# Optimization experiments

Hardware: AMD Instinct MI355X
Metric: run time of the kernel (lower is better)

## Reference

```python
import jax, jax.numpy as jnp
import numpy as np

IMSIZE = 128; R = 2; B = 2; C = 3; D = 64; Q = 128; M = 8; ITERS = 32
N = IMSIZE * IMSIZE
EPS = 1e-8


def _build_edges(S, r):
    # local (2r+1)^2 pixel neighborhood, as in build_perception(imsize, perception_size)
    ys, xs = np.meshgrid(np.arange(S), np.arange(S), indexing='ij')
    rows, cols = [], []
    for dy in range(-r, r + 1):
        for dx in range(-r, r + 1):
            ny, nx = ys + dy, xs + dx
            ok = (ny >= 0) & (ny < S) & (nx >= 0) & (nx < S)
            rows.append((ys * S + xs)[ok])
            cols.append((ny * S + nx)[ok])
    return (np.concatenate(rows).astype(np.int32), np.concatenate(cols).astype(np.int32))


def _conv(x, w, b=None):
    y = jax.lax.conv_general_dilated(x, w, (1, 1), 'SAME', dimension_numbers=('NHWC', 'HWIO', 'NHWC'))
    return y if b is None else y + b


def _bn(x, g, b):
    mu = x.mean((0, 1, 2))
    var = x.var((0, 1, 2))
    return (x - mu) * jax.lax.rsqrt(var + 1e-5) * g + b


def _resblock(f, w1, g1, t1, w2, g2, t2):
    h = jax.nn.relu(_bn(_conv(f, w1), g1, t1))
    h = _bn(_conv(h, w2), g2, t2)
    return jax.nn.relu(f + h)


def _forward(x, w_bb1, b_bb1, w_bb2, b_bb2,
             w_k1, g_k1, t_k1, w_k2, g_k2, t_k2, w_kp, b_kp,
             w_q1, g_q1, t_q1, w_q2, g_q2, t_q2, w_qp,
             h0, row, col, agent_idx):
    # conv backbone (preserves spatial resolution)
    f = jax.nn.relu(_conv(x, w_bb1, b_bb1))
    f = jax.nn.relu(_conv(f, w_bb2, b_bb2))
    # key / query heads: ResidualBlock + 1x1 conv
    ks = _conv(_resblock(f, w_k1, g_k1, t_k1, w_k2, g_k2, t_k2), w_kp, b_kp).reshape(B, N, D)
    qs = _conv(_resblock(f, w_q1, g_q1, t_q1, w_q2, g_q2, t_q2), w_qp).reshape(B, N, D)
    # edge-gather cosine similarity (torch.cosine_similarity with eps=1e-8)
    qe = qs[:, row]          # [B, E, D]
    ke = ks[:, col]          # [B, E, D]
    weights = (qe * ke).sum(-1) / (
        jnp.maximum(jnp.linalg.norm(qe, axis=-1), EPS) *
        jnp.maximum(jnp.linalg.norm(ke, axis=-1), EPS))   # [B, E]

    # 32-iteration sparse adjacency propagation: h <- normalize(A @ h)
    def step(h, _):
        msg = jnp.zeros_like(h).at[:, row, :].add(weights[:, :, None] * h[:, col, :])
        h = msg / jnp.maximum(jnp.linalg.norm(msg, axis=-1, keepdims=True), EPS)
        return h, None

    h, _ = jax.lax.scan(step, h0, None, length=ITERS)     # [B, N, Q]

    # competition routing: pixels compete for M agent slots via cosine affinity
    pix = h / jnp.maximum(jnp.linalg.norm(h, axis=-1, keepdims=True), EPS)
    ag = pix[:, agent_idx]                                # [B, M, Q]
    sim = jnp.einsum('bnq,bmq->bnm', pix, ag)
    masks = jax.nn.softmax(sim * 10.0, axis=-1)           # [B, N, M]
    return masks.reshape(B, IMSIZE, IMSIZE, M).transpose(0, 3, 1, 2)  # [B, M, W, H]


def setup_inputs() -> dict:
    key = jax.random.key(0)
    k = jax.random.split(key, 12)
    s = 0.05
    row, col = _build_edges(IMSIZE, R)
    agent_idx = np.linspace(0, N - 1, M).astype(np.int32)
    return dict(
        x=jax.random.normal(k[0], (B, IMSIZE, IMSIZE, C), jnp.float32),
        w_bb1=jax.random.normal(k[1], (3, 3, C, D), jnp.float32) * s, b_bb1=jnp.zeros((D,), jnp.float32),
        w_bb2=jax.random.normal(k[2], (3, 3, D, D), jnp.float32) * s, b_bb2=jnp.zeros((D,), jnp.float32),
        w_k1=jax.random.normal(k[3], (3, 3, D, D), jnp.float32) * s,
        g_k1=jnp.ones((D,), jnp.float32), t_k1=jnp.zeros((D,), jnp.float32),
        w_k2=jax.random.normal(k[4], (3, 3, D, D), jnp.float32) * s,
        g_k2=jnp.ones((D,), jnp.float32), t_k2=jnp.zeros((D,), jnp.float32),
        w_kp=jax.random.normal(k[5], (1, 1, D, D), jnp.float32) * s, b_kp=jnp.zeros((D,), jnp.float32),
        w_q1=jax.random.normal(k[6], (3, 3, D, D), jnp.float32) * s,
        g_q1=jnp.ones((D,), jnp.float32), t_q1=jnp.zeros((D,), jnp.float32),
        w_q2=jax.random.normal(k[7], (3, 3, D, D), jnp.float32) * s,
        g_q2=jnp.ones((D,), jnp.float32), t_q2=jnp.zeros((D,), jnp.float32),
        w_qp=jax.random.normal(k[8], (1, 1, D, D), jnp.float32) * s,
        h0=jax.random.normal(k[9], (B, N, Q), jnp.float32),
        row=jnp.asarray(row), col=jnp.asarray(col),
        agent_idx=jnp.asarray(agent_idx),
    )


def reference(x, w_bb1, b_bb1, w_bb2, b_bb2,
              w_k1, g_k1, t_k1, w_k2, g_k2, t_k2, w_kp, b_kp,
              w_q1, g_q1, t_q1, w_q2, g_q2, t_q2, w_qp,
              h0, row, col, agent_idx):
    return _forward(x, w_bb1, b_bb1, w_bb2, b_bb2,
                    w_k1, g_k1, t_k1, w_k2, g_k2, t_k2, w_kp, b_kp,
                    w_q1, g_q1, t_q1, w_q2, g_q2, t_q2, w_qp,
                    h0, row, col, agent_idx)
```

## Files before the change

### kernel.cpp

```cpp
#include <hip/hip_runtime.h>
#include <math.h>

#define NPIX 16384
#define EPSF 1e-8f

typedef float f32x4 __attribute__((ext_vector_type(4)));
typedef short s16x8 __attribute__((ext_vector_type(8)));

__device__ __forceinline__ float wred64(float s){
  s += __shfl_xor(s, 32); s += __shfl_xor(s, 16); s += __shfl_xor(s, 8);
  s += __shfl_xor(s, 4);  s += __shfl_xor(s, 2);  s += __shfl_xor(s, 1);
  return s;
}
__device__ __forceinline__ float rdlane(float v, int l){
  return __int_as_float(__builtin_amdgcn_readlane(__float_as_int(v), l));
}
__device__ __forceinline__ float dot4f(float4 a, float4 b, float acc){
  acc = fmaf(a.x,b.x,acc); acc = fmaf(a.y,b.y,acc);
  acc = fmaf(a.z,b.z,acc); acc = fmaf(a.w,b.w,acc);
  return acc;
}
__device__ __forceinline__ void bf16split(float v, unsigned short &hi, unsigned short &lo){
  unsigned u = __float_as_uint(v);
  unsigned r = u + 0x7FFFu + ((u >> 16) & 1u);
  hi = (unsigned short)(r >> 16);
  float hf = __uint_as_float(((unsigned)hi) << 16);
  float l = v - hf;
  unsigned u2 = __float_as_uint(l);
  unsigned r2 = u2 + 0x7FFFu + ((u2 >> 16) & 1u);
  lo = (unsigned short)(r2 >> 16);
}

__global__ __launch_bounds__(256) void prep_kernel(const float* __restrict__ w_bb2, const float* __restrict__ w_k1,
                            const float* __restrict__ w_k2, const float* __restrict__ w_q1,
                            const float* __restrict__ w_q2, const float* __restrict__ w_kp,
                            const float* __restrict__ w_qp, unsigned short* __restrict__ wh,
                            unsigned short* __restrict__ wl, float* __restrict__ wtp,
                            float* __restrict__ stats){
  int gid = blockIdx.x*256 + threadIdx.x;
  if (gid < 184320){
    int j = gid & 7;
    int t1 = gid >> 3;
    int lane = t1 & 63;
    int t2 = t1 >> 6;
    int kb = t2 % 18;
    int t3 = t2 / 18;
    int ct = t3 & 3;
    int c  = t3 >> 2;
    const float* src = c==0? w_bb2 : c==1? w_k1 : c==2? w_k2 : c==3? w_q1 : w_q2;
    int cout = ct*16 + (lane & 15);
    int k = kb*32 + (lane>>4)*8 + j;
    float v = src[k*64 + cout];
    unsigned short h,l; bf16split(v,h,l);
    wh[gid] = h; wl[gid] = l;
  } else if (gid < 192512){
    int t = gid - 184320; int which = t >> 12; int d = t & 4095;
    const float* src = which ? w_qp : w_kp;
    int k = d & 3, cout = (d>>2) & 63, cin4 = d >> 8;
    wtp[t] = src[(cin4*4 + k)*64 + cout];
  } else if (gid < 193024){
    stats[gid - 192512] = 0.f;
  }
}

__global__ __launch_bounds__(256) void conv1_kernel(const float* __restrict__ x, const float* __restrict__ w,
                                                    const float* __restrict__ bias, float* __restrict__ out){
  int wv = blockIdx.x*4 + (threadIdx.x >> 6);
  int c  = threadIdx.x & 63;
  int p0 = wv << 3;
  int ub = __builtin_amdgcn_readfirstlane(p0);
  int b  = ub >> 14; int i0 = ub & (NPIX-1);
  int y  = i0 >> 7, x0 = i0 & 127;
  float wv_[9][3];
  #pragma unroll
  for (int t=0;t<9;++t)
    #pragma unroll
    for (int ci=0;ci<3;++ci) wv_[t][ci] = w[(t*3+ci)*64 + c];
  float bv = bias[c];
  float acc[8];
  #pragma unroll
  for (int p=0;p<8;++p) acc[p] = bv;
  for (int ky=0; ky<3; ++ky){
    int ny = y + ky - 1;
    if ((unsigned)ny >= 128u) continue;
    const float* rowp = x + ((b<<14) + ny*128)*3;
    for (int kx=0; kx<3; ++kx){
      int t = ky*3 + kx;
      #pragma unroll
      for (int p=0;p<8;++p){
        int col = x0 + p + kx - 1;
        if ((unsigned)col < 128u){
          const float* ip = rowp + col*3;
          acc[p] = fmaf(ip[0], wv_[t][0], acc[p]);
          acc[p] = fmaf(ip[1], wv_[t][1], acc[p]);
          acc[p] = fmaf(ip[2], wv_[t][2], acc[p]);
        }
      }
    }
  }
  float* op = out + (p0 << 6) + c;
  #pragma unroll
  for (int p=0;p<8;++p) op[p*64] = fmaxf(acc[p], 0.f);
}

__global__ __launch_bounds__(512) void conv3m_kernel(const float* __restrict__ in,
    const unsigned short* __restrict__ wh, const unsigned short* __restrict__ wl,
    const float* __restrict__ bias, int relu,
    const float* __restrict__ bnst, const float* __restrict__ bng, const float* __restrict__ bnb,
    float* __restrict__ out){
  __shared__ unsigned short lhi[12672];
  __shared__ unsigned short llo[12672];
  __shared__ float lout[4352];
  __shared__ float la[64], lb[64];
  int blk = blockIdx.x;
  int xh = blk & 1, y = (blk>>1) & 127, b = blk >> 8;
  int x0 = xh << 6;
  int tid = threadIdx.x;
  if (tid < 64){
    float a = 1.f, bo = 0.f;
    if (bnst){
      float mu  = bnst[tid] * (1.f/32768.f);
      float var = bnst[64+tid] * (1.f/32768.f) - mu*mu;
      a  = bng[tid] * rsqrtf(var + 1e-5f);
      bo = bnb[tid] - mu*a;
    }
    la[tid] = a; lb[tid] = bo;
  }
  __syncthreads();
  for (int s = tid; s < 3168; s += 512){
    int pr = s >> 4, cq = s & 15;
    int ky = pr / 66, px = pr - ky*66;
    int ny = y + ky - 1, gx = x0 - 1 + px;
    float v0=0.f, v1=0.f, v2=0.f, v3=0.f;
    if ((unsigned)ny < 128u && (unsigned)gx < 128u){
      const float* ip = in + (((b<<14) + ny*128 + gx)<<6) + (cq<<2);
      float4 t = *(const float4*)ip;
      int c0 = cq<<2;
      v0 = fmaxf(fmaf(t.x, la[c0],   lb[c0]),   0.f);
      v1 = fmaxf(fmaf(t.y, la[c0+1], lb[c0+1]), 0.f);
      v2 = fmaxf(fmaf(t.z, la[c0+2], lb[c0+2]), 0.f);
      v3 = fmaxf(fmaf(t.w, la[c0+3], lb[c0+3]), 0.f);
    }
    unsigned short h0,l0,h1,l1,h2,l2,h3,l3;
    bf16split(v0,h0,l0); bf16split(v1,h1,l1); bf16split(v2,h2,l2); bf16split(v3,h3,l3);
    int slot = (cq >> 1) ^ (pr & 7);
    int byte = pr*128 + (slot<<4) + ((cq & 1) << 3);
    *(uint2*)((char*)lhi + byte) = make_uint2((unsigned)h0 | ((unsigned)h1<<16),
                                              (unsigned)h2 | ((unsigned)h3<<16));
    *(uint2*)((char*)llo + byte) = make_uint2((unsigned)l0 | ((unsigned)l1<<16),
                                              (unsigned)l2 | ((unsigned)l3<<16));
  }
  __syncthreads();
  int lane = tid & 63, wid = tid >> 6;
  int pxsub = wid & 3, ch = wid >> 2;
  int col16 = lane & 15, kgrp = lane >> 4;
  f32x4 acc0 = {0.f,0.f,0.f,0.f}, acc1 = acc0, acl0 = acc0, acl1 = acc0;
  int abase = (ch*2*18)*512 + lane*8;
  #pragma unroll
  for (int kb=0; kb<18; ++kb){
    int tap = kb >> 1;
    int ky = (tap >= 6) ? 2 : (tap >= 3 ? 1 : 0);
    int kx = tap - ky*3;
    int pr = ky*66 + pxsub*16 + col16 + kx;
    int ci0 = ((kb & 1) << 5) + (kgrp << 3);
    int byte = pr*128 + ((((ci0 >> 3) ^ (pr & 7))) << 4);
    s16x8 Bh = *(const s16x8*)((const char*)lhi + byte);
    s16x8 Bl = *(const s16x8*)((const char*)llo + byte);
    int ao = abase + kb*512;
    s16x8 Ah0 = *(const s16x8*)(wh + ao);
    s16x8 Al0 = *(const s16x8*)(wl + ao);
    s16x8 Ah1 = *(const s16x8*)(wh + ao + 9216);
    s16x8 Al1 = *(const s16x8*)(wl + ao + 9216);
    acc0 = __builtin_amdgcn_mfma_f32_16x16x32_bf16(Ah0, Bh, acc0, 0, 0, 0);
    acl0 = __builtin_amdgcn_mfma_f32_16x16x32_bf16(Ah0, Bl, acl0, 0, 0, 0);
    acc1 = __builtin_amdgcn_mfma_f32_16x16x32_bf16(Ah1, Bh, acc1, 0, 0, 0);
    acl1 = __builtin_amdgcn_mfma_f32_16x16x32_bf16(Ah1, Bl, acl1, 0, 0, 0);
    acl0 = __builtin_amdgcn_mfma_f32_16x16x32_bf16(Al0, Bh, acl0, 0, 0, 0);
    acl1 = __builtin_amdgcn_mfma_f32_16x16x32_bf16(Al1, Bh, acl1, 0, 0, 0);
  }
  acc0 = acc0 + acl0;
  acc1 = acc1 + acl1;
  int pxl = pxsub*16 + col16;
  int co0 = ch*32 + kgrp*4;
  *(f32x4*)(lout + pxl*68 + co0)      = acc0;
  *(f32x4*)(lout + pxl*68 + co0 + 16) = acc1;
  __syncthreads();
  {
    int px = tid >> 3, c8 = (tid & 7) << 3;
    const float* lp = lout + px*68 + c8;
    float r0[8];
    #pragma unroll
    for (int j=0;j<8;++j) r0[j] = lp[j];
    if (bias){
      #pragma unroll
      for (int j=0;j<8;++j) r0[j] += bias[c8+j];
    }
    if (relu){
      #pragma unroll
      for (int j=0;j<8;++j) r0[j] = fmaxf(r0[j], 0.f);
    }
    float* op = out + (((b<<14) + y*128 + x0 + px)<<6) + c8;
    #pragma unroll
    for (int j=0;j<8;++j) op[j] = r0[j];
  }
}

__global__ __launch_bounds__(256) void stats_kernel(const float* __restrict__ t, float* __restrict__ stats){
  __shared__ float s1[64], s2[64];
  int tid = threadIdx.x;
  if (tid < 64){ s1[tid] = 0.f; s2[tid] = 0.f; }
  __syncthreads();
  int gid = blockIdx.x*256 + tid;
  float sum = 0.f, ss = 0.f;
  for (int idx = gid; idx < 2097152; idx += 131072){
    float v = t[idx]; sum += v; ss += v*v;
  }
  int c = gid & 63;
  atomicAdd(&s1[c], sum);
  atomicAdd(&s2[c], ss);
  __syncthreads();
  if (tid < 64){ atomicAdd(&stats[tid], s1[tid]); atomicAdd(&stats[64+tid], s2[tid]); }
}

__global__ __launch_bounds__(256) void resfuse_kernel(float* __restrict__ t, const float* __restrict__ f,
                                                      const float* __restrict__ stats, const float* __restrict__ g,
                                                      const float* __restrict__ beta){
  int idx4 = blockIdx.x*256 + threadIdx.x;
  float4 v = ((float4*)t)[idx4];
  float4 fv = ((const float4*)f)[idx4];
  int c0 = (idx4 & 15) * 4;
  float a[4], bb[4];
  #pragma unroll
  for (int j=0;j<4;++j){
    int c = c0 + j;
    float mu  = stats[c]    * (1.f/32768.f);
    float var = stats[64+c] * (1.f/32768.f) - mu*mu;
    a[j]  = g[c] * rsqrtf(var + 1e-5f);
    bb[j] = beta[c] - mu*a[j];
  }
  v.x = fmaxf(fv.x + fmaf(v.x, a[0], bb[0]), 0.f);
  v.y = fmaxf(fv.y + fmaf(v.y, a[1], bb[1]), 0.f);
  v.z = fmaxf(fv.z + fmaf(v.z, a[2], bb[2]), 0.f);
  v.w = fmaxf(fv.w + fmaf(v.w, a[3], bb[3]), 0.f);
  ((float4*)t)[idx4] = v;
}

__global__ __launch_bounds__(256) void proj_kernel(const float* __restrict__ r, const float* __restrict__ wt1,
                                                   const float* __restrict__ bias, float* __restrict__ out,
                                                   float* __restrict__ nrm){
  int wv = blockIdx.x*4 + (threadIdx.x >> 6);
  int c  = threadIdx.x & 63;
  int p0 = wv << 3;
  int ub = __builtin_amdgcn_readfirstlane(p0);
  const float4* wq = (const float4*)wt1 + c;
  float4 w[16];
  #pragma unroll
  for (int q=0;q<16;++q) w[q] = wq[q*64];
  float bv = bias ? bias[c] : 0.f;
  #pragma unroll
  for (int p=0;p<8;++p){
    const float* ip = r + ((ub + p) << 6);
    float a0 = bv, a1 = 0.f;
    #pragma unroll
    for (int q=0;q<16;q+=2){
      float4 i0 = *(const float4*)(ip + (q<<2));
      float4 i1 = *(const float4*)(ip + ((q+1)<<2));
      a0 = dot4f(i0, w[q],   a0);
      a1 = dot4f(i1, w[q+1], a1);
    }
    float acc = a0 + a1;
    out[((p0+p)<<6) + c] = acc;
    float s = wred64(acc*acc);
    if (c == 0) nrm[p0+p] = sqrtf(s);
  }
}

#define EW_PAD 68
__global__ __launch_bounds__(256) void edge_kernel(const float* __restrict__ qs, const float* __restrict__ ks,
                                                   const float* __restrict__ nq, const float* __restrict__ nk,
                                                   float* __restrict__ W){
  __shared__ float klds[100*EW_PAD];
  __shared__ float qlds[16*EW_PAD];
  int blk = blockIdx.x;
  int b = blk >> 10; int rem = blk & 1023;
  int y = rem >> 3; int x0 = (rem & 7) << 4;
  int tid = threadIdx.x;
  for (int s = tid; s < 1600; s += 256){
    int cin4 = s & 15; int col = (s >> 4) % 20; int r = (s >> 4) / 20;
    int ry = y - 2 + r; ry = ry < 0 ? 0 : (ry > 127 ? 127 : ry);
    int cx = x0 - 2 + col; cx = cx < 0 ? 0 : (cx > 127 ? 127 : cx);
    float4 v = *(const float4*)(ks + (((b<<14) + ry*128 + cx)<<6) + cin4*4);
    *(float4*)(klds + (r*20+col)*EW_PAD + cin4*4) = v;
  }
  {
    int cin4 = tid & 15; int px = tid >> 4;
    float4 v = *(const float4*)(qs + (((b<<14) + y*128 + x0 + px)<<6) + cin4*4);
    *(float4*)(qlds + px*EW_PAD + cin4*4) = v;
  }
  __syncthreads();
  #pragma unroll
  for (int pair=0; pair<2; ++pair){
    int t2 = tid + pair*256;
    int px = t2 >> 5; int o = t2 & 31;
    if (o < 25){
      int dy = o/5 - 2, dx = o%5 - 2;
      int yy = y + dy, xx = x0 + px + dx;
      bool valid = ((unsigned)yy < 128u) && ((unsigned)xx < 128u);
      const float* kq = klds + ((dy+2)*20 + (px+dx+2))*EW_PAD;
      const float* qq = qlds + px*EW_PAD;
      float a0 = 0.f, a1 = 0.f;
      #pragma unroll
      for (int q=0; q<16; q+=2){
        a0 = dot4f(*(const float4*)(qq + q*4),     *(const float4*)(kq + q*4),     a0);
        a1 = dot4f(*(const float4*)(qq + (q+1)*4), *(const float4*)(kq + (q+1)*4), a1);
      }
      float acc = a0 + a1;
      int gp = (b<<14) + y*128 + x0 + px;
      float wv_ = 0.f;
      if (valid){
        int gj = (b<<14) + yy*128 + xx;
        float rq = 1.f / fmaxf(nq[gp], EPSF);
        float rk = 1.f / fmaxf(nk[gj], EPSF);
        wv_ = acc * rq * rk;
      }
      W[gp*25 + o] = wv_;
    }
  }
}

__global__ __launch_bounds__(256) void mp_iter_kernel(const float* __restrict__ src, float* __restrict__ dst,
                                                      const float* __restrict__ W){
  int lane = threadIdx.x & 63;
  int wid  = threadIdx.x >> 6;
  int blk  = blockIdx.x;
  int xcd = blk & 7, s = blk >> 3;
  int row_id = xcd*32 + (s >> 2);
  int q4 = s & 3;
  int b = row_id >> 7, y = row_id & 127;
  int x0 = ((q4 << 2) + wid) << 3;
  int gp0 = (b << 14) + y*128 + x0;
  int lo = lane < 25 ? lane : 24;
  float wv[8];
  #pragma unroll
  for (int p=0;p<8;++p) wv[p] = W[(gp0+p)*25 + lo];
  const float* rp[5];
  #pragma unroll
  for (int r=0;r<5;++r){
    int ry = y - 2 + r; ry = ry < 0 ? 0 : (ry > 127 ? 127 : ry);
    rp[r] = src + (((b<<14) + ry*128) << 7) + lane;
  }
  float wa[5][5], wb[5][5];
  #pragma unroll
  for (int cc=0; cc<4; ++cc){
    int xc = x0 - 2 + cc; if (xc < 0) xc = 0;
    int off = xc << 7;
    #pragma unroll
    for (int r=0;r<5;++r){ wa[r][cc] = rp[r][off]; wb[r][cc] = rp[r][off + 64]; }
  }
  #pragma unroll
  for (int p=0;p<8;++p){
    int xl = x0 + p + 2; if (xl > 127) xl = 127;
    int off = xl << 7;
    #pragma unroll
    for (int r=0;r<5;++r){ wa[r][4] = rp[r][off]; wb[r][4] = rp[r][off + 64]; }
    float a0 = 0.f, a1 = 0.f;
    #pragma unroll
    for (int r=0;r<5;++r){
      #pragma unroll
      for (int cc=0;cc<5;++cc){
        float w = rdlane(wv[p], r*5+cc);
        a0 = fmaf(w, wa[r][cc], a0);
        a1 = fmaf(w, wb[r][cc], a1);
      }
    }
    float ss = wred64(a0*a0 + a1*a1);
    float sc = 1.f / fmaxf(sqrtf(ss), EPSF);
    float* dp = dst + ((gp0 + p) << 7) + lane;
    dp[0] = a0*sc; dp[64] = a1*sc;
    #pragma unroll
    for (int r=0;r<5;++r){
      #pragma unroll
      for (int cc=0;cc<4;++cc){ wa[r][cc] = wa[r][cc+1]; wb[r][cc] = wb[r][cc+1]; }
    }
  }
}

__global__ void mp_agents_kernel(const float* __restrict__ hf, const int* __restrict__ agidx,
                                 float* __restrict__ agbuf){
  int lane = threadIdx.x & 63; int w = threadIdx.x >> 6;
  int ab = w >> 3, m = w & 7;
  int ai = agidx[m];
  const float* hp = hf + (((ab<<14) + ai) << 7) + lane;
  float v0 = hp[0], v1 = hp[64];
  float ss = wred64(v0*v0 + v1*v1);
  float sc = 1.f / fmaxf(sqrtf(ss), EPSF);
  float* ap = agbuf + (((ab<<3) + m) << 7) + lane;
  ap[0] = v0*sc; ap[64] = v1*sc;
}

__global__ __launch_bounds__(256) void mp_final_kernel(const float* __restrict__ hf, const float* __restrict__ agbuf,
                                                       float* __restrict__ out){
  int lane = threadIdx.x & 63;
  int wid  = threadIdx.x >> 6;
  int blk  = blockIdx.x;
  int xcd = blk & 7, s = blk >> 3;
  int row_id = xcd*32 + (s >> 2);
  int q4 = s & 3;
  int b = row_id >> 7, y = row_id & 127;
  int x0 = ((q4 << 2) + wid) << 3;
  int gp0 = (b << 14) + y*128 + x0;
  #pragma unroll 1
  for (int p=0;p<8;++p){
    int gp = gp0 + p;
    const float* hp = hf + (gp << 7) + lane;
    float v0 = hp[0], v1 = hp[64];
    float ss = wred64(v0*v0 + v1*v1);
    float sc = 1.f / fmaxf(sqrtf(ss), EPSF);
    float p0 = v0*sc, p1 = v1*sc;
    float sim[8];
    #pragma unroll
    for (int m=0;m<8;++m){
      const float* ap = agbuf + (((b<<3) + m) << 7) + lane;
      sim[m] = wred64(p0*ap[0] + p1*ap[64]);
    }
    float mx = sim[0];
    #pragma unroll
    for (int m=1;m<8;++m) mx = fmaxf(mx, sim[m]);
    float e[8]; float sum = 0.f;
    #pragma unroll
    for (int m=0;m<8;++m){ e[m] = __expf((sim[m]-mx)*10.f); sum += e[m]; }
    float rs = 1.f / sum;
    if (lane < 8){
      float val = e[0];
      #pragma unroll
      for (int m=1;m<8;++m) val = (lane==m) ? e[m] : val;
      out[(((b<<3)+lane)<<14) + y*128 + x0 + p] = val * rs;
    }
  }
}

extern "C" void kernel_launch(void* const* d_in, const int* in_sizes, int n_in,
                              void* d_out, int out_size, void* d_ws, size_t ws_size,
                              hipStream_t stream) {
  (void)in_sizes; (void)n_in; (void)out_size; (void)ws_size;
  const float* x     = (const float*)d_in[0];
  const float* w_bb1 = (const float*)d_in[1];
  const float* b_bb1 = (const float*)d_in[2];
  const float* w_bb2 = (const float*)d_in[3];
  const float* b_bb2 = (const float*)d_in[4];
  const float* w_k1  = (const float*)d_in[5];
  const float* g_k1  = (const float*)d_in[6];
  const float* t_k1  = (const float*)d_in[7];
  const float* w_k2  = (const float*)d_in[8];
  const float* g_k2  = (const float*)d_in[9];
  const float* t_k2  = (const float*)d_in[10];
  const float* w_kp  = (const float*)d_in[11];
  const float* b_kp  = (const float*)d_in[12];
  const float* w_q1  = (const float*)d_in[13];
  const float* g_q1  = (const float*)d_in[14];
  const float* t_q1  = (const float*)d_in[15];
  const float* w_q2  = (const float*)d_in[16];
  const float* g_q2  = (const float*)d_in[17];
  const float* t_q2  = (const float*)d_in[18];
  const float* w_qp  = (const float*)d_in[19];
  const float* h0    = (const float*)d_in[20];
  const int*   agidx = (const int*)d_in[23];
  float* out = (float*)d_out;
  float* ws  = (float*)d_ws;

  float* S0 = ws + 0;
  float* S1 = ws + 2097152;
  float* S2 = ws + 4194304;
  float* S3 = ws + 6291456;
  float* S4 = ws + 8388608;
  float* WW = ws + 12582912;
  float* NK = ws + 13402112;
  float* NQ = ws + 13434880;
  float* ST = ws + 13467648;
  float* AG = ws + 13468160;
  float* WTp = ws + 13470208;
  unsigned short* WH = (unsigned short*)(ws + 13478400);
  unsigned short* WL = WH + 184320;
  float* HA = ws + 0;
  float* HB = ws + 4194304;

  prep_kernel<<<754, 256, 0, stream>>>(w_bb2, w_k1, w_k2, w_q1, w_q2, w_kp, w_qp, WH, WL, WTp, ST);
  conv1_kernel<<<1024, 256, 0, stream>>>(x, w_bb1, b_bb1, S0);
  conv3m_kernel<<<512, 512, 0, stream>>>(S0, WH + 0, WL + 0, b_bb2, 1, nullptr, nullptr, nullptr, S1);
  conv3m_kernel<<<512, 512, 0, stream>>>(S1, WH + 36864, WL + 36864, nullptr, 0, nullptr, nullptr, nullptr, S2);
  stats_kernel<<<512, 256, 0, stream>>>(S2, ST + 0);
  conv3m_kernel<<<512, 512, 0, stream>>>(S1, WH + 3*36864, WL + 3*36864, nullptr, 0, nullptr, nullptr, nullptr, S3);
  stats_kernel<<<512, 256, 0, stream>>>(S3, ST + 256);
  conv3m_kernel<<<512, 512, 0, stream>>>(S2, WH + 2*36864, WL + 2*36864, nullptr, 0, ST + 0, g_k1, t_k1, S0);
  stats_kernel<<<512, 256, 0, stream>>>(S0, ST + 128);
  resfuse_kernel<<<2048, 256, 0, stream>>>(S0, S1, ST + 128, g_k2, t_k2);
  proj_kernel<<<1024, 256, 0, stream>>>(S0, WTp + 0, b_kp, S4, NK);
  conv3m_kernel<<<512, 512, 0, stream>>>(S3, WH + 4*36864, WL + 4*36864, nullptr, 0, ST + 256, g_q1, t_q1, S2);
  stats_kernel<<<512, 256, 0, stream>>>(S2, ST + 384);
  resfuse_kernel<<<2048, 256, 0, stream>>>(S2, S1, ST + 384, g_q2, t_q2);
  proj_kernel<<<1024, 256, 0, stream>>>(S2, WTp + 4096, nullptr, S3, NQ);
  edge_kernel<<<2048, 256, 0, stream>>>(S3, S4, NQ, NK, WW);
  const float* sbuf = h0;
  for (int it = 0; it < 32; ++it){
    float* dbuf = (it & 1) ? HB : HA;
    mp_iter_kernel<<<1024, 256, 0, stream>>>(sbuf, dbuf, WW);
    sbuf = dbuf;
  }
  mp_agents_kernel<<<1, 1024, 0, stream>>>(HB, agidx, AG);
  mp_final_kernel<<<1024, 256, 0, stream>>>(HB, AG, out);
}
```

Measured before the change: 662.4 us.

## Fuse BN stats into conv epilogue and run propagation as one cooperative kernel

The BatchNorm statistics reduction moves into the conv3m epilogue through warp shuffles and LDS atomics, which drops four separate stats kernels that re-read whole tensors. The 32 propagation launches plus the agent and final kernels become a single cooperative kernel that syncs the grid between iterations. Each block keeps its edge weights in registers across iterations and covers 16 pixels per wave instead of 8. The trade-offs are 32 grid-wide barriers, higher register pressure, and a fallback to the old multi-launch path if the cooperative launch fails.

```diff
diff --git a/kernel.cpp b/kernel.cpp
--- a/kernel.cpp
+++ b/kernel.cpp
@@ -1,5 +1,8 @@
 #include <hip/hip_runtime.h>
+#include <hip/hip_cooperative_groups.h>
 #include <math.h>
+
+namespace cg = cooperative_groups;
 
 #define NPIX 16384
 #define EPSF 1e-8f
@@ -107,11 +110,12 @@
     const unsigned short* __restrict__ wh, const unsigned short* __restrict__ wl,
     const float* __restrict__ bias, int relu,
     const float* __restrict__ bnst, const float* __restrict__ bng, const float* __restrict__ bnb,
-    float* __restrict__ out){
+    float* __restrict__ out, float* __restrict__ ost){
   __shared__ unsigned short lhi[12672];
   __shared__ unsigned short llo[12672];
   __shared__ float lout[4352];
   __shared__ float la[64], lb[64];
+  __shared__ float ls1[64], ls2[64];
   int blk = blockIdx.x;
   int xh = blk & 1, y = (blk>>1) & 127, b = blk >> 8;
   int x0 = xh << 6;
@@ -125,6 +129,7 @@
       bo = bnb[tid] - mu*a;
     }
     la[tid] = a; lb[tid] = bo;
+    ls1[tid] = 0.f; ls2[tid] = 0.f;
   }
   __syncthreads();
   for (int s = tid; s < 3168; s += 512){
@@ -202,24 +207,25 @@
     float* op = out + (((b<<14) + y*128 + x0 + px)<<6) + c8;
     #pragma unroll
     for (int j=0;j<8;++j) op[j] = r0[j];
-  }
-}
-
-__global__ __launch_bounds__(256) void stats_kernel(const float* __restrict__ t, float* __restrict__ stats){
-  __shared__ float s1[64], s2[64];
-  int tid = threadIdx.x;
-  if (tid < 64){ s1[tid] = 0.f; s2[tid] = 0.f; }
-  __syncthreads();
-  int gid = blockIdx.x*256 + tid;
-  float sum = 0.f, ss = 0.f;
-  for (int idx = gid; idx < 2097152; idx += 131072){
-    float v = t[idx]; sum += v; ss += v*v;
-  }
-  int c = gid & 63;
-  atomicAdd(&s1[c], sum);
-  atomicAdd(&s2[c], ss);
-  __syncthreads();
-  if (tid < 64){ atomicAdd(&stats[tid], s1[tid]); atomicAdd(&stats[64+tid], s2[tid]); }
+    if (ost){
+      float s1v[8], s2v[8];
+      #pragma unroll
+      for (int j=0;j<8;++j){ s1v[j] = r0[j]; s2v[j] = r0[j]*r0[j]; }
+      #pragma unroll
+      for (int m=8; m<64; m<<=1){
+        #pragma unroll
+        for (int j=0;j<8;++j){ s1v[j] += __shfl_xor(s1v[j], m); s2v[j] += __shfl_xor(s2v[j], m); }
+      }
+      int lane2 = tid & 63;
+      if ((lane2 >> 3) == 0){
+        int c0 = (lane2 & 7) << 3;
+        #pragma unroll
+        for (int j=0;j<8;++j){ atomicAdd(&ls1[c0+j], s1v[j]); atomicAdd(&ls2[c0+j], s2v[j]); }
+      }
+      __syncthreads();
+      if (tid < 64){ atomicAdd(&ost[tid], ls1[tid]); atomicAdd(&ost[64+tid], ls2[tid]); }
+    }
+  }
 }
 
 __global__ __launch_bounds__(256) void resfuse_kernel(float* __restrict__ t, const float* __restrict__ f,
@@ -324,6 +330,108 @@
         wv_ = acc * rq * rk;
       }
       W[gp*25 + o] = wv_;
+    }
+  }
+}
+
+__global__ __launch_bounds__(256) void mp_fused_kernel(const float* __restrict__ h0,
+    float* __restrict__ HA, float* __restrict__ HB, const float* __restrict__ W,
+    const int* __restrict__ agidx, float* __restrict__ out){
+  cg::grid_group grid = cg::this_grid();
+  int lane = threadIdx.x & 63;
+  int wid  = threadIdx.x >> 6;
+  int blk  = blockIdx.x;
+  int xcd = blk & 7, s = blk >> 3;
+  int row_id = xcd*32 + (s >> 1);
+  int half = s & 1;
+  int b = row_id >> 7, y = row_id & 127;
+  int x0 = half*64 + wid*16;
+  int gp0 = (b << 14) + y*128 + x0;
+  int lo = lane < 25 ? lane : 24;
+  float wv[16];
+  #pragma unroll
+  for (int p=0;p<16;++p) wv[p] = W[(gp0+p)*25 + lo];
+  int rowoff[5];
+  #pragma unroll
+  for (int r=0;r<5;++r){
+    int ry = y - 2 + r; ry = ry < 0 ? 0 : (ry > 127 ? 127 : ry);
+    rowoff[r] = (((b<<14) + ry*128) << 7) + lane;
+  }
+  const float* src = h0;
+  float* dst = HA;
+  #pragma unroll 1
+  for (int it = 0; it < 32; ++it){
+    float wa[5][5], wb[5][5];
+    #pragma unroll
+    for (int cc=0; cc<4; ++cc){
+      int xc = x0 - 2 + cc; if (xc < 0) xc = 0;
+      int off = xc << 7;
+      #pragma unroll
+      for (int r=0;r<5;++r){ const float* rp = src + rowoff[r]; wa[r][cc] = rp[off]; wb[r][cc] = rp[off + 64]; }
+    }
+    #pragma unroll 2
+    for (int p=0;p<16;++p){
+      int xl = x0 + p + 2; if (xl > 127) xl = 127;
+      int off = xl << 7;
+      #pragma unroll
+      for (int r=0;r<5;++r){ const float* rp = src + rowoff[r]; wa[r][4] = rp[off]; wb[r][4] = rp[off + 64]; }
+      float a0 = 0.f, a1 = 0.f;
+      #pragma unroll
+      for (int r=0;r<5;++r){
+        #pragma unroll
+        for (int cc=0;cc<5;++cc){
+          float w = rdlane(wv[p], r*5+cc);
+          a0 = fmaf(w, wa[r][cc], a0);
+          a1 = fmaf(w, wb[r][cc], a1);
+        }
+      }
+      float ss = wred64(a0*a0 + a1*a1);
+      float sc = 1.f / fmaxf(sqrtf(ss), EPSF);
+      float* dp = dst + ((gp0 + p) << 7) + lane;
+      dp[0] = a0*sc; dp[64] = a1*sc;
+      #pragma unroll
+      for (int r=0;r<5;++r){
+        #pragma unroll
+        for (int cc=0;cc<4;++cc){ wa[r][cc] = wa[r][cc+1]; wb[r][cc] = wb[r][cc+1]; }
+      }
+    }
+    grid.sync();
+    src = dst;
+    dst = (it & 1) ? HA : HB;
+  }
+  float av0[8], av1[8], isc[8];
+  #pragma unroll
+  for (int m=0;m<8;++m){
+    int ai = agidx[m];
+    const float* ap = src + (((b<<14) + ai) << 7) + lane;
+    av0[m] = ap[0]; av1[m] = ap[64];
+    float ssm = wred64(av0[m]*av0[m] + av1[m]*av1[m]);
+    isc[m] = 1.f / fmaxf(sqrtf(ssm), EPSF);
+  }
+  #pragma unroll 1
+  for (int p=0;p<16;++p){
+    int gp = gp0 + p;
+    const float* hp = src + (gp << 7) + lane;
+    float v0 = hp[0], v1 = hp[64];
+    float ss = wred64(v0*v0 + v1*v1);
+    float sc = 1.f / fmaxf(sqrtf(ss), EPSF);
+    float p0 = v0*sc, p1 = v1*sc;
+    float sim[8];
+    #pragma unroll
+    for (int m=0;m<8;++m)
+      sim[m] = wred64(p0*av0[m] + p1*av1[m]) * isc[m];
+    float mx = sim[0];
+    #pragma unroll
+    for (int m=1;m<8;++m) mx = fmaxf(mx, sim[m]);
+    float e[8]; float sum = 0.f;
+    #pragma unroll
+    for (int m=0;m<8;++m){ e[m] = __expf((sim[m]-mx)*10.f); sum += e[m]; }
+    float rs = 1.f / sum;
+    if (lane < 8){
+      float val = e[0];
+      #pragma unroll
+      for (int m=1;m<8;++m) val = (lane==m) ? e[m] : val;
+      out[(((b<<3)+lane)<<14) + y*128 + x0 + p] = val * rs;
     }
   }
 }
@@ -486,26 +594,31 @@
 
   prep_kernel<<<754, 256, 0, stream>>>(w_bb2, w_k1, w_k2, w_q1, w_q2, w_kp, w_qp, WH, WL, WTp, ST);
   conv1_kernel<<<1024, 256, 0, stream>>>(x, w_bb1, b_bb1, S0);
-  conv3m_kernel<<<512, 512, 0, stream>>>(S0, WH + 0, WL + 0, b_bb2, 1, nullptr, nullptr, nullptr, S1);
-  conv3m_kernel<<<512, 512, 0, stream>>>(S1, WH + 36864, WL + 36864, nullptr, 0, nullptr, nullptr, nullptr, S2);
-  stats_kernel<<<512, 256, 0, stream>>>(S2, ST + 0);
-  conv3m_kernel<<<512, 512, 0, stream>>>(S1, WH + 3*36864, WL + 3*36864, nullptr, 0, nullptr, nullptr, nullptr, S3);
-  stats_kernel<<<512, 256, 0, stream>>>(S3, ST + 256);
-  conv3m_kernel<<<512, 512, 0, stream>>>(S2, WH + 2*36864, WL + 2*36864, nullptr, 0, ST + 0, g_k1, t_k1, S0);
-  stats_kernel<<<512, 256, 0, stream>>>(S0, ST + 128);
+  conv3m_kernel<<<512, 512, 0, stream>>>(S0, WH + 0, WL + 0, b_bb2, 1, nullptr, nullptr, nullptr, S1, nullptr);
+  conv3m_kernel<<<512, 512, 0, stream>>>(S1, WH + 36864, WL + 36864, nullptr, 0, nullptr, nullptr, nullptr, S2, ST + 0);
+  conv3m_kernel<<<512, 512, 0, stream>>>(S1, WH + 3*36864, WL + 3*36864, nullptr, 0, nullptr, nullptr, nullptr, S3, ST + 256);
+  conv3m_kernel<<<512, 512, 0, stream>>>(S2, WH + 2*36864, WL + 2*36864, nullptr, 0, ST + 0, g_k1, t_k1, S0, ST + 128);
   resfuse_kernel<<<2048, 256, 0, stream>>>(S0, S1, ST + 128, g_k2, t_k2);
   proj_kernel<<<1024, 256, 0, stream>>>(S0, WTp + 0, b_kp, S4, NK);
-  conv3m_kernel<<<512, 512, 0, stream>>>(S3, WH + 4*36864, WL + 4*36864, nullptr, 0, ST + 256, g_q1, t_q1, S2);
-  stats_kernel<<<512, 256, 0, stream>>>(S2, ST + 384);
+  conv3m_kernel<<<512, 512, 0, stream>>>(S3, WH + 4*36864, WL + 4*36864, nullptr, 0, ST + 256, g_q1, t_q1, S2, ST + 384);
   resfuse_kernel<<<2048, 256, 0, stream>>>(S2, S1, ST + 384, g_q2, t_q2);
   proj_kernel<<<1024, 256, 0, stream>>>(S2, WTp + 4096, nullptr, S3, NQ);
   edge_kernel<<<2048, 256, 0, stream>>>(S3, S4, NQ, NK, WW);
-  const float* sbuf = h0;
-  for (int it = 0; it < 32; ++it){
-    float* dbuf = (it & 1) ? HB : HA;
-    mp_iter_kernel<<<1024, 256, 0, stream>>>(sbuf, dbuf, WW);
-    sbuf = dbuf;
-  }
-  mp_agents_kernel<<<1, 1024, 0, stream>>>(HB, agidx, AG);
-  mp_final_kernel<<<1024, 256, 0, stream>>>(HB, AG, out);
-}
+  {
+    const float* h0p = h0; float* HAp = HA; float* HBp = HB;
+    const float* WWp = WW; const int* agp = agidx; float* outp = out;
+    void* args[] = { (void*)&h0p, (void*)&HAp, (void*)&HBp, (void*)&WWp, (void*)&agp, (void*)&outp };
+    hipError_t rc = hipLaunchCooperativeKernel((const void*)mp_fused_kernel,
+                                               dim3(512), dim3(256), args, 0, stream);
+    if (rc != hipSuccess){
+      const float* sbuf = h0;
+      for (int it = 0; it < 32; ++it){
+        float* dbuf = (it & 1) ? HB : HA;
+        mp_iter_kernel<<<1024, 256, 0, stream>>>(sbuf, dbuf, WW);
+        sbuf = dbuf;
+      }
+      mp_agents_kernel<<<1, 1024, 0, stream>>>(HB, agidx, AG);
+      mp_final_kernel<<<1024, 256, 0, stream>>>(HB, AG, out);
+    }
+  }
+}
```

After: 2.513 ms. 279% more time.
